# Optimization experiments

Hardware: AMD Instinct MI355X
Metric: run time of the kernel (lower is better)

Reference implementation:

```python
import jax, jax.numpy as jnp
import numpy as np

N_NODES = 20000
NC = 16
NUM_BASIS = 5
MAX_CENTER = 3.5

# Real-basis Clebsch-Gordan tensors C[m, m_f, m_o] for the (l, l_f) -> l_o paths.
# Real l=1 basis ordered (m=-1,0,1) = (y,z,x); (y,z,x) is a cyclic permutation of
# (x,y,z) so the standard Levi-Civita gives the 1x1->1 coupling.
_C000 = np.ones((1, 1, 1), dtype=np.float32)
_C011 = np.eye(3, dtype=np.float32).reshape(1, 3, 3)
_C101 = np.eye(3, dtype=np.float32).reshape(3, 1, 3)
_C110 = (np.eye(3, dtype=np.float32) / np.sqrt(3.0)).reshape(3, 3, 1)
_eps = np.zeros((3, 3, 3), dtype=np.float32)
for (i, j, k) in [(0, 1, 2), (1, 2, 0), (2, 0, 1)]:
    _eps[i, j, k] = 1.0
    _eps[i, k, j] = -1.0
_C111 = (_eps / np.sqrt(2.0)).astype(np.float32)

Y00 = 0.28209479177387814  # 1 / (2 sqrt(pi))
Y1C = 0.4886025119029199   # sqrt(3 / (4 pi))


def _spherical_filter(edges, coeffs, l_f):
    """SphericalFilter.__call__: RBF radial part x solid harmonics. -> [E, n_c, 2l_f+1]."""
    centers = jnp.linspace(0.0, MAX_CENTER, NUM_BASIS)
    spread = (MAX_CENTER - 0.0) / NUM_BASIS  # (max - min) / num_basis = 0.7
    radius = jnp.linalg.norm(edges, ord=2, axis=-1)              # [E]
    rbfs = jnp.exp(-spread * (radius[:, None] - centers) ** 2)   # [E, num_basis]
    rad = rbfs @ coeffs.T                                        # [E, n_c]
    if l_f == 0:
        y = jnp.full(edges.shape[:-1] + (1,), Y00, dtype=edges.dtype)
    else:  # l_f == 1: solid harmonics r^1 * Y_1m, order (y, z, x)
        y = Y1C * edges[:, jnp.array([1, 2, 0])]
    y = jnp.nan_to_num(y)
    return rad[:, :, None] * y[:, None, :]


def _tp(nodes, filt, cg, w):
    """Depthwise CG tensor product: [E,c,m],[E,c,f],[m,f,o] -> w[c] * [E,c,o]."""
    out = jnp.einsum('ecm,ecf,mfo->eco', nodes, filt, jnp.asarray(cg))
    return w[None, :, None] * out


def setup_inputs() -> dict:
    key = jax.random.key(0)
    ks = jax.random.split(key, 16)
    E = 640000
    inp = {
        'coords': jax.random.normal(ks[0], (N_NODES, 3), dtype=jnp.float32),
        'nodes0': jax.random.normal(ks[1], (N_NODES, NC, 1), dtype=jnp.float32),
        'nodes1': jax.random.normal(ks[2], (N_NODES, NC, 3), dtype=jnp.float32),
        'edges': jax.random.normal(ks[3], (E, 3), dtype=jnp.float32),
        'senders': jax.random.randint(ks[4], (E,), 0, N_NODES, dtype=jnp.int32),
        'receivers': jax.random.randint(ks[5], (E,), 0, N_NODES, dtype=jnp.int32),
        'coeffs_00': jax.random.uniform(ks[6], (NC, NUM_BASIS), dtype=jnp.float32),
        'coeffs_01': jax.random.uniform(ks[7], (NC, NUM_BASIS), dtype=jnp.float32),
        'coeffs_10': jax.random.uniform(ks[8], (NC, NUM_BASIS), dtype=jnp.float32),
        'coeffs_11': jax.random.uniform(ks[9], (NC, NUM_BASIS), dtype=jnp.float32),
        'w_000': jax.random.normal(ks[10], (NC,), dtype=jnp.float32) + 1.0,
        'w_011': jax.random.normal(ks[11], (NC,), dtype=jnp.float32) + 1.0,
        'w_101': jax.random.normal(ks[12], (NC,), dtype=jnp.float32) + 1.0,
        'w_110': jax.random.normal(ks[13], (NC,), dtype=jnp.float32) + 1.0,
        'w_111': jax.random.normal(ks[14], (NC,), dtype=jnp.float32) + 1.0,
    }
    return inp


def reference(coords, nodes0, nodes1, edges, senders, receivers,
              coeffs_00, coeffs_01, coeffs_10, coeffs_11,
              w_000, w_011, w_101, w_110, w_111):
    # Gather sender node features once per l.
    n0s = nodes0[senders]  # [E, NC, 1]
    n1s = nodes1[senders]  # [E, NC, 3]

    # Filters (loop order: l=0 filters [l_f=0, l_f=1], then l=1 filters).
    f00 = _spherical_filter(edges, coeffs_00, 0)  # [E, NC, 1]
    f01 = _spherical_filter(edges, coeffs_01, 1)  # [E, NC, 3]
    f10 = _spherical_filter(edges, coeffs_10, 0)  # [E, NC, 1]
    f11 = _spherical_filter(edges, coeffs_11, 1)  # [E, NC, 3]

    # Tensor-product messages, concatenated per output degree along channels.
    # l_o = 0 paths: (l=0, l_f=0), (l=1, l_f=1)
    m0 = jnp.concatenate([
        _tp(n0s, f00, _C000, w_000),
        _tp(n1s, f11, _C110, w_110),
    ], axis=-2)  # [E, 2*NC, 1]
    # l_o = 1 paths: (0,1), (1,0), (1,1)
    m1 = jnp.concatenate([
        _tp(n0s, f01, _C011, w_011),
        _tp(n1s, f10, _C101, w_101),
        _tp(n1s, f11, _C111, w_111),
    ], axis=-2)  # [E, 3*NC, 3]

    new0 = jax.ops.segment_sum(m0, receivers, num_segments=N_NODES)
    new1 = jax.ops.segment_sum(m1, receivers, num_segments=N_NODES)
    return coords, new0, new1
```

## Files before the change

### kernel.cpp

```cpp
#include <hip/hip_runtime.h>

#define E_EDGES 640000
#define NN 20000
#define NC 16
#define PBIN 64

#define Y00F 0.28209479177387814f
#define Y1CF 0.4886025119029199f
#define RS3  0.5773502691896258f
#define RS2  0.7071067811865476f

typedef float nf4 __attribute__((ext_vector_type(4)));

struct Acc {
    float a000, a110;
    float a011x, a011y, a011z;
    float a101x, a101y, a101z;
    float a111x, a111y, a111z;
};


__global__ void init1_kernel(const float* __restrict__ coords,
                             float* __restrict__ out,
                             int* __restrict__ cnt,
                             int* __restrict__ ovf_count) {
    int i = blockIdx.x * blockDim.x + threadIdx.x;
    if (i < 3 * NN) out[i] = coords[i];
    if (i < NN) cnt[i] = 0;
    if (i == 0) *ovf_count = 0;
}

__global__ void bin_kernel(const float* __restrict__ edges,
                           const int* __restrict__ senders,
                           const int* __restrict__ receivers,
                           int* __restrict__ cnt,
                           nf4* __restrict__ bins,
                           int* __restrict__ ovf_count,
                           int* __restrict__ ovf_list) {
    int e = blockIdx.x * blockDim.x + threadIdx.x;
    if (e >= E_EDGES) return;
    float ex = edges[3 * e + 0];
    float ey = edges[3 * e + 1];
    float ez = edges[3 * e + 2];
    int s  = senders[e];
    int rc = receivers[e];
    int pos = atomicAdd(&cnt[rc], 1);
    if (pos < PBIN) {
        float r2 = ex * ex + ey * ey + ez * ez;
        float r  = sqrtf(r2);
        float A  = __expf(-0.7f * r2);
        float t  = __expf(1.225f * r);
        nf4 r0 = {Y1CF * ey, Y1CF * ez, Y1CF * ex, __int_as_float(s)};
        nf4 r1 = {A, t, 0.0f, 0.0f};
        nf4* p = bins + 2 * ((size_t)rc * PBIN + pos);
        p[0] = r0;
        p[1] = r1;
    } else {
        int k = atomicAdd(ovf_count, 1);
        if (k < 4096) ovf_list[k] = e;
    }
}

__global__ __launch_bounds__(256) void gather1_kernel(
    const nf4*    __restrict__ bins,
    const int*    __restrict__ cnt,
    const float*  __restrict__ nodes0,
    const float*  __restrict__ nodes1,
    const float*  __restrict__ c00, const float* __restrict__ c01,
    const float*  __restrict__ c10, const float* __restrict__ c11,
    const float*  __restrict__ w000, const float* __restrict__ w011,
    const float*  __restrict__ w101, const float* __restrict__ w110,
    const float*  __restrict__ w111,
    float* __restrict__ out0, float* __restrict__ out1)
{
    int gtid = blockIdx.x * blockDim.x + threadIdx.x;
    int node = gtid >> 6;
    int lane = threadIdx.x & 63;
    int c    = lane & 15;
    int j    = lane >> 4;
    if (node >= NN) return;

    const float KB[5] = {1.0f, 0.58512723f, 0.11721218f, 0.00803909f, 1.8876652e-4f};
    float k00[5], k01[5], k10[5], k11[5];
#pragma unroll
    for (int b = 0; b < 5; b++) {
        k00[b] = c00[c * 5 + b] * KB[b];
        k01[b] = c01[c * 5 + b] * KB[b];
        k10[b] = c10[c * 5 + b] * KB[b];
        k11[b] = c11[c * 5 + b] * KB[b];
    }

    int n = cnt[node];
    n = (n < PBIN) ? n : PBIN;
    const nf4* base = bins + 2 * (size_t)node * PBIN;

    Acc A = {};

#define HORNER(k, t) fmaf((t), fmaf((t), fmaf((t), fmaf((t), k[4], k[3]), k[2]), k[1]), k[0])
#define BODY(r0, r1)                                                       \
    {                                                                      \
        int s = __float_as_int(r0.w);                                      \
        float Af = r1.x, tf = r1.y;                                        \
        float rad00 = Af * HORNER(k00, tf);                                \
        float rad01 = Af * HORNER(k01, tf);                                \
        float rad10 = Af * HORNER(k10, tf);                                \
        float rad11 = Af * HORNER(k11, tf);                                \
        float n0 = nodes0[s * NC + c];                                     \
        const float* n1p = nodes1 + (s * NC + c) * 3;                      \
        float n1a = n1p[0], n1b = n1p[1], n1c = n1p[2];                    \
        float py = r0.x, pz = r0.y, px = r0.z;                             \
        A.a000 = fmaf(n0, rad00, A.a000);                                  \
        A.a110 = fmaf(rad11, n1a * py + n1b * pz + n1c * px, A.a110);      \
        float kA = n0 * rad01;                                             \
        A.a011x = fmaf(kA, py, A.a011x);                                   \
        A.a011y = fmaf(kA, pz, A.a011y);                                   \
        A.a011z = fmaf(kA, px, A.a011z);                                   \
        A.a101x = fmaf(rad10, n1a, A.a101x);                               \
        A.a101y = fmaf(rad10, n1b, A.a101y);                               \
        A.a101z = fmaf(rad10, n1c, A.a101z);                               \
        A.a111x = fmaf(rad11, n1b * px - n1c * pz, A.a111x);               \
        A.a111y = fmaf(rad11, n1c * py - n1a * px, A.a111y);               \
        A.a111z = fmaf(rad11, n1a * pz - n1b * py, A.a111z);               \
    }

    int i = j;
    for (; i + 4 < n; i += 8) {
        nf4 a0 = __builtin_nontemporal_load(&base[2 * i]);
        nf4 a1 = __builtin_nontemporal_load(&base[2 * i + 1]);
        nf4 b0 = __builtin_nontemporal_load(&base[2 * (i + 4)]);
        nf4 b1 = __builtin_nontemporal_load(&base[2 * (i + 4) + 1]);
        BODY(a0, a1);
        BODY(b0, b1);
    }
    if (i < n) {
        nf4 a0 = __builtin_nontemporal_load(&base[2 * i]);
        nf4 a1 = __builtin_nontemporal_load(&base[2 * i + 1]);
        BODY(a0, a1);
    }
#undef BODY
#undef HORNER

#define RED(v) v += __shfl_xor(v, 16, 64); v += __shfl_xor(v, 32, 64)
    RED(A.a000); RED(A.a110);
    RED(A.a011x); RED(A.a011y); RED(A.a011z);
    RED(A.a101x); RED(A.a101y); RED(A.a101z);
    RED(A.a111x); RED(A.a111y); RED(A.a111z);
#undef RED

    if (j == 0) {
        float s000 = w000[c] * Y00F;
        float s110 = w110[c] * RS3;
        float s011 = w011[c];
        float s101 = w101[c] * Y00F;
        float s111 = w111[c] * RS2;

        out0[node * 32 + c]      = s000 * A.a000;
        out0[node * 32 + 16 + c] = s110 * A.a110;

        float* o1 = out1 + node * 144;
        o1[3 * c + 0] = s011 * A.a011x;
        o1[3 * c + 1] = s011 * A.a011y;
        o1[3 * c + 2] = s011 * A.a011z;
        o1[3 * (16 + c) + 0] = s101 * A.a101x;
        o1[3 * (16 + c) + 1] = s101 * A.a101y;
        o1[3 * (16 + c) + 2] = s101 * A.a101z;
        o1[3 * (32 + c) + 0] = s111 * A.a111x;
        o1[3 * (32 + c) + 1] = s111 * A.a111y;
        o1[3 * (32 + c) + 2] = s111 * A.a111z;
    }
}

__global__ void cleanup_kernel(
    const int* __restrict__ ovf_count, const int* __restrict__ ovf_list,
    const float* __restrict__ edges, const int* __restrict__ senders,
    const int* __restrict__ receivers,
    const float* __restrict__ nodes0, const float* __restrict__ nodes1,
    const float* __restrict__ c00, const float* __restrict__ c01,
    const float* __restrict__ c10, const float* __restrict__ c11,
    const float* __restrict__ w000, const float* __restrict__ w011,
    const float* __restrict__ w101, const float* __restrict__ w110,
    const float* __restrict__ w111,
    float* __restrict__ out0, float* __restrict__ out1)
{
    int nov = *ovf_count;
    if (nov > 4096) nov = 4096;
    for (int k = threadIdx.x; k < nov; k += blockDim.x) {
        int e = ovf_list[k];
        float ex = edges[3 * e + 0], ey = edges[3 * e + 1], ez = edges[3 * e + 2];
        float r = sqrtf(ex * ex + ey * ey + ez * ez);
        float rbf[5];
#pragma unroll
        for (int b = 0; b < 5; b++) {
            float d = r - 0.875f * (float)b;
            rbf[b] = __expf(-0.7f * d * d);
        }
        int s = senders[e], rc = receivers[e];
        const float* n0p = nodes0 + s * NC;
        const float* n1p = nodes1 + s * NC * 3;
        float* o0 = out0 + rc * 32;
        float* o1 = out1 + rc * 144;
        float pey = Y1CF * ey, pez = Y1CF * ez, pex = Y1CF * ex;
        for (int c = 0; c < NC; c++) {
            float rad00 = 0.f, rad01 = 0.f, rad10 = 0.f, rad11 = 0.f;
#pragma unroll
            for (int b = 0; b < 5; b++) {
                rad00 = fmaf(rbf[b], c00[c * 5 + b], rad00);
                rad01 = fmaf(rbf[b], c01[c * 5 + b], rad01);
                rad10 = fmaf(rbf[b], c10[c * 5 + b], rad10);
                rad11 = fmaf(rbf[b], c11[c * 5 + b], rad11);
            }
            float n0 = n0p[c];
            float n1a = n1p[3 * c + 0], n1b = n1p[3 * c + 1], n1c = n1p[3 * c + 2];
            float f11a = rad11 * pey, f11b = rad11 * pez, f11c = rad11 * pex;
            atomicAdd(&o0[c], w000[c] * n0 * rad00 * Y00F);
            atomicAdd(&o0[16 + c], w110[c] * RS3 * (n1a * f11a + n1b * f11b + n1c * f11c));
            float kA = w011[c] * n0 * rad01;
            atomicAdd(&o1[3 * c + 0], kA * pey);
            atomicAdd(&o1[3 * c + 1], kA * pez);
            atomicAdd(&o1[3 * c + 2], kA * pex);
            float kB = w101[c] * rad10 * Y00F;
            atomicAdd(&o1[3 * (16 + c) + 0], kB * n1a);
            atomicAdd(&o1[3 * (16 + c) + 1], kB * n1b);
            atomicAdd(&o1[3 * (16 + c) + 2], kB * n1c);
            float kC = w111[c] * RS2;
            atomicAdd(&o1[3 * (32 + c) + 0], kC * (n1b * f11c - n1c * f11b));
            atomicAdd(&o1[3 * (32 + c) + 1], kC * (n1c * f11a - n1a * f11c));
            atomicAdd(&o1[3 * (32 + c) + 2], kC * (n1a * f11b - n1b * f11a));
        }
    }
}

__global__ void init_out_fb(const float* __restrict__ coords,
                            float* __restrict__ out, int out_size) {
    int i = blockIdx.x * blockDim.x + threadIdx.x;
    if (i < 3 * NN) out[i] = coords[i];
    else if (i < out_size) out[i] = 0.0f;
}

__global__ __launch_bounds__(256) void tp_edges_fb(
    const float* __restrict__ edges, const int* __restrict__ senders,
    const int* __restrict__ receivers, const float* __restrict__ nodes0,
    const float* __restrict__ nodes1,
    const float* __restrict__ c00, const float* __restrict__ c01,
    const float* __restrict__ c10, const float* __restrict__ c11,
    const float* __restrict__ w000, const float* __restrict__ w011,
    const float* __restrict__ w101, const float* __restrict__ w110,
    const float* __restrict__ w111,
    float* __restrict__ out0, float* __restrict__ out1) {
    int e = blockIdx.x * blockDim.x + threadIdx.x;
    if (e >= E_EDGES) return;
    float ex = edges[3 * e + 0], ey = edges[3 * e + 1], ez = edges[3 * e + 2];
    float r = sqrtf(ex * ex + ey * ey + ez * ez);
    float rbf[5];
#pragma unroll
    for (int b = 0; b < 5; b++) {
        float d = r - 0.875f * (float)b;
        rbf[b] = __expf(-0.7f * d * d);
    }
    int s = senders[e], rc = receivers[e];
    const float* n0p = nodes0 + s * NC;
    const float* n1p = nodes1 + s * NC * 3;
    float* o0 = out0 + rc * 32;
    float* o1 = out1 + rc * 144;
    float pey = Y1CF * ey, pez = Y1CF * ez, pex = Y1CF * ex;
    for (int c = 0; c < NC; c++) {
        float rad00 = 0.f, rad01 = 0.f, rad10 = 0.f, rad11 = 0.f;
#pragma unroll
        for (int b = 0; b < 5; b++) {
            rad00 = fmaf(rbf[b], c00[c * 5 + b], rad00);
            rad01 = fmaf(rbf[b], c01[c * 5 + b], rad01);
            rad10 = fmaf(rbf[b], c10[c * 5 + b], rad10);
            rad11 = fmaf(rbf[b], c11[c * 5 + b], rad11);
        }
        float n0 = n0p[c];
        float n1a = n1p[3 * c + 0], n1b = n1p[3 * c + 1], n1c = n1p[3 * c + 2];
        float f11a = rad11 * pey, f11b = rad11 * pez, f11c = rad11 * pex;
        atomicAdd(&o0[c], w000[c] * n0 * rad00 * Y00F);
        atomicAdd(&o0[16 + c], w110[c] * RS3 * (n1a * f11a + n1b * f11b + n1c * f11c));
        float kA = w011[c] * n0 * rad01;
        atomicAdd(&o1[3 * c + 0], kA * pey);
        atomicAdd(&o1[3 * c + 1], kA * pez);
        atomicAdd(&o1[3 * c + 2], kA * pex);
        float kB = w101[c] * rad10 * Y00F;
        atomicAdd(&o1[3 * (16 + c) + 0], kB * n1a);
        atomicAdd(&o1[3 * (16 + c) + 1], kB * n1b);
        atomicAdd(&o1[3 * (16 + c) + 2], kB * n1c);
        float kC = w111[c] * RS2;
        atomicAdd(&o1[3 * (32 + c) + 0], kC * (n1b * f11c - n1c * f11b));
        atomicAdd(&o1[3 * (32 + c) + 1], kC * (n1c * f11a - n1a * f11c));
        atomicAdd(&o1[3 * (32 + c) + 2], kC * (n1a * f11b - n1b * f11a));
    }
}

extern "C" void kernel_launch(void* const* d_in, const int* in_sizes, int n_in,
                              void* d_out, int out_size, void* d_ws, size_t ws_size,
                              hipStream_t stream) {
    const float* coords    = (const float*)d_in[0];
    const float* nodes0    = (const float*)d_in[1];
    const float* nodes1    = (const float*)d_in[2];
    const float* edges     = (const float*)d_in[3];
    const int*   senders   = (const int*)  d_in[4];
    const int*   receivers = (const int*)  d_in[5];
    const float* c00       = (const float*)d_in[6];
    const float* c01       = (const float*)d_in[7];
    const float* c10       = (const float*)d_in[8];
    const float* c11       = (const float*)d_in[9];
    const float* w000      = (const float*)d_in[10];
    const float* w011      = (const float*)d_in[11];
    const float* w101      = (const float*)d_in[12];
    const float* w110      = (const float*)d_in[13];
    const float* w111      = (const float*)d_in[14];

    float* out  = (float*)d_out;
    float* out0 = out + 3 * NN;
    float* out1 = out + 3 * NN + NN * 2 * NC;

    size_t bins_bytes = (size_t)NN * PBIN * 32;
    size_t need1 = bins_bytes + (size_t)(NN + 1 + 4096) * 4;

    if (ws_size >= need1) {
        nf4* bins      = (nf4*)d_ws;
        int* cnt       = (int*)((char*)d_ws + bins_bytes);
        int* ovf_count = cnt + NN;
        int* ovf_list  = ovf_count + 1;

        init1_kernel<<<(3 * NN + 255) / 256, 256, 0, stream>>>(coords, out, cnt, ovf_count);
        bin_kernel<<<(E_EDGES + 255) / 256, 256, 0, stream>>>(
            edges, senders, receivers, cnt, bins, ovf_count, ovf_list);
        gather1_kernel<<<(NN * 64 + 255) / 256, 256, 0, stream>>>(
            bins, cnt, nodes0, nodes1,
            c00, c01, c10, c11, w000, w011, w101, w110, w111, out0, out1);
        cleanup_kernel<<<1, 256, 0, stream>>>(
            ovf_count, ovf_list, edges, senders, receivers, nodes0, nodes1,
            c00, c01, c10, c11, w000, w011, w101, w110, w111, out0, out1);
    } else {
        init_out_fb<<<(out_size + 255) / 256, 256, 0, stream>>>(coords, out, out_size);
        tp_edges_fb<<<(E_EDGES + 255) / 256, 256, 0, stream>>>(
            edges, senders, receivers, nodes0, nodes1,
            c00, c01, c10, c11, w000, w011, w101, w110, w111, out0, out1);
    }
}
```

Before: 179.8 us.

## Pack per-edge bin records into 16 bytes using fp16 geometry and basis term

Result: faster. 173.5 us (-3.5%).

```diff
diff --git a/kernel.cpp b/kernel.cpp
--- a/kernel.cpp
+++ b/kernel.cpp
@@ -1,4 +1,5 @@
 #include <hip/hip_runtime.h>
+#include <hip/hip_fp16.h>
 
 #define E_EDGES 640000
 #define NN 20000
@@ -18,6 +19,18 @@
     float a101x, a101y, a101z;
     float a111x, a111y, a111z;
 };
+
+__device__ __forceinline__ unsigned pack2h(float a, float b) {
+    unsigned short ua = __half_as_ushort(__float2half(a));
+    unsigned short ub = __half_as_ushort(__float2half(b));
+    return (unsigned)ua | ((unsigned)ub << 16);
+}
+__device__ __forceinline__ float lo_h(unsigned u) {
+    return __half2float(__ushort_as_half((unsigned short)(u & 0xffffu)));
+}
+__device__ __forceinline__ float hi_h(unsigned u) {
+    return __half2float(__ushort_as_half((unsigned short)(u >> 16)));
+}
 
 
 __global__ void init1_kernel(const float* __restrict__ coords,
@@ -50,11 +63,12 @@
         float r  = sqrtf(r2);
         float A  = __expf(-0.7f * r2);
         float t  = __expf(1.225f * r);
-        nf4 r0 = {Y1CF * ey, Y1CF * ez, Y1CF * ex, __int_as_float(s)};
-        nf4 r1 = {A, t, 0.0f, 0.0f};
-        nf4* p = bins + 2 * ((size_t)rc * PBIN + pos);
-        p[0] = r0;
-        p[1] = r1;
+        nf4 rec;
+        rec.x = __uint_as_float(pack2h(Y1CF * ey, Y1CF * ez));
+        rec.y = __uint_as_float(pack2h(Y1CF * ex, t));
+        rec.z = A;
+        rec.w = __int_as_float(s);
+        bins[(size_t)rc * PBIN + pos] = rec;
     } else {
         int k = atomicAdd(ovf_count, 1);
         if (k < 4096) ovf_list[k] = e;
@@ -92,15 +106,19 @@
 
     int n = cnt[node];
     n = (n < PBIN) ? n : PBIN;
-    const nf4* base = bins + 2 * (size_t)node * PBIN;
+    const nf4* base = bins + (size_t)node * PBIN;
 
     Acc A = {};
 
 #define HORNER(k, t) fmaf((t), fmaf((t), fmaf((t), fmaf((t), k[4], k[3]), k[2]), k[1]), k[0])
-#define BODY(r0, r1)                                                       \
+#define BODY(rec)                                                          \
     {                                                                      \
-        int s = __float_as_int(r0.w);                                      \
-        float Af = r1.x, tf = r1.y;                                        \
+        unsigned u0 = __float_as_uint(rec.x);                              \
+        unsigned u1 = __float_as_uint(rec.y);                              \
+        float py = lo_h(u0), pz = hi_h(u0);                                \
+        float px = lo_h(u1), tf = hi_h(u1);                                \
+        float Af = rec.z;                                                  \
+        int s = __float_as_int(rec.w);                                     \
         float rad00 = Af * HORNER(k00, tf);                                \
         float rad01 = Af * HORNER(k01, tf);                                \
         float rad10 = Af * HORNER(k10, tf);                                \
@@ -108,7 +126,6 @@
         float n0 = nodes0[s * NC + c];                                     \
         const float* n1p = nodes1 + (s * NC + c) * 3;                      \
         float n1a = n1p[0], n1b = n1p[1], n1c = n1p[2];                    \
-        float py = r0.x, pz = r0.y, px = r0.z;                             \
         A.a000 = fmaf(n0, rad00, A.a000);                                  \
         A.a110 = fmaf(rad11, n1a * py + n1b * pz + n1c * px, A.a110);      \
         float kA = n0 * rad01;                                             \
@@ -124,18 +141,19 @@
     }
 
     int i = j;
-    for (; i + 4 < n; i += 8) {
-        nf4 a0 = __builtin_nontemporal_load(&base[2 * i]);
-        nf4 a1 = __builtin_nontemporal_load(&base[2 * i + 1]);
-        nf4 b0 = __builtin_nontemporal_load(&base[2 * (i + 4)]);
-        nf4 b1 = __builtin_nontemporal_load(&base[2 * (i + 4) + 1]);
-        BODY(a0, a1);
-        BODY(b0, b1);
-    }
-    if (i < n) {
-        nf4 a0 = __builtin_nontemporal_load(&base[2 * i]);
-        nf4 a1 = __builtin_nontemporal_load(&base[2 * i + 1]);
-        BODY(a0, a1);
+    for (; i + 12 < n; i += 16) {
+        nf4 r0 = __builtin_nontemporal_load(&base[i]);
+        nf4 r1 = __builtin_nontemporal_load(&base[i + 4]);
+        nf4 r2 = __builtin_nontemporal_load(&base[i + 8]);
+        nf4 r3 = __builtin_nontemporal_load(&base[i + 12]);
+        BODY(r0);
+        BODY(r1);
+        BODY(r2);
+        BODY(r3);
+    }
+    for (; i < n; i += 4) {
+        nf4 r0 = __builtin_nontemporal_load(&base[i]);
+        BODY(r0);
     }
 #undef BODY
 #undef HORNER
@@ -315,7 +333,7 @@
     float* out0 = out + 3 * NN;
     float* out1 = out + 3 * NN + NN * 2 * NC;
 
-    size_t bins_bytes = (size_t)NN * PBIN * 32;
+    size_t bins_bytes = (size_t)NN * PBIN * 16;
     size_t need1 = bins_bytes + (size_t)(NN + 1 + 4096) * 4;
 
     if (ws_size >= need1) {
```
